# Performance work log

Measured on AMD Instinct MI355X. Metric: run time of the kernel, lower is better.

## Reference

```python
import jax, jax.numpy as jnp
import numpy as np

B, T, C, HS = 1024, 128, 384, 64


def setup_inputs() -> dict:
    key = jax.random.key(0)
    k1, k2, k3, k4 = jax.random.split(key, 4)
    std = 1.0 / np.sqrt(C)  # ~ nn.Linear default init scale
    return {
        "x": jax.random.normal(k1, (B, T, C), dtype=jnp.float32),
        "Wq": jax.random.normal(k2, (C, HS), dtype=jnp.float32) * std,
        "Wk": jax.random.normal(k3, (C, HS), dtype=jnp.float32) * std,
        "Wv": jax.random.normal(k4, (C, HS), dtype=jnp.float32) * std,
    }


def reference(x, Wq, Wk, Wv):
    # x: [B, T, C]; Wq/Wk/Wv: [C, HS]
    q = jnp.einsum("btc,ch->bth", x, Wq)
    k = jnp.einsum("btc,ch->bth", x, Wk)
    v = jnp.einsum("btc,ch->bth", x, Wv)
    scale = 1.0 / jnp.sqrt(jnp.asarray(k.shape[-1], dtype=x.dtype))
    wei = jnp.einsum("bth,bsh->bts", q, k) * scale  # [B, T, T]
    t = x.shape[1]
    causal = jnp.tril(jnp.ones((t, t), dtype=bool))
    wei = jnp.where(causal, wei, jnp.asarray(-jnp.inf, dtype=wei.dtype))
    wei = jax.nn.softmax(wei, axis=-1)
    # dropout omitted (eval mode / deterministic reference)
    out = jnp.einsum("bts,bsh->bth", wei, v)  # [B, T, HS]
    return out
```

## Files before the change

### kernel.cpp

```cpp
#include <hip/hip_runtime.h>


typedef __attribute__((ext_vector_type(8)))  short  short8;
typedef __attribute__((ext_vector_type(16))) float  floatx16;
typedef __attribute__((ext_vector_type(4)))  float  float4v;

#define T_DIM   128
#define C_DIM   384
#define HS      64
#define NCHUNK  12
#define SLAB    1536

#define QK_PITCH 68
#define V_PITCH  132
#define P_PITCH  132
#define Q_OFF 0
#define K_OFF 17408
#define V_OFF 34816
#define LDS_BYTES 51712
#define P_OFF 0
#define XS_OFF 0
#define XS_BUF 16384

#define MFMA(a,b,c) __builtin_amdgcn_mfma_f32_32x32x16_bf16((a),(b),(c),0,0,0)

__device__ inline unsigned short f2bf(float f){
    unsigned u = __builtin_bit_cast(unsigned, f);
    u += 0x7FFFu + ((u >> 16) & 1u);
    return (unsigned short)(u >> 16);
}

__device__ inline short8 ld_b64x2(const char* p){
    union { unsigned long long u[2]; short8 s; } r;
    r.u[0] = *(const unsigned long long*)(p);
    r.u[1] = *(const unsigned long long*)(p + 8);
    return r.s;
}

__global__ void prep_wt(const float* __restrict__ Wq, const float* __restrict__ Wk,
                        const float* __restrict__ Wv, unsigned short* __restrict__ wt){
    int idx = blockIdx.x * 256 + threadIdx.x;
    if (idx >= 48 * SLAB) return;
    int slab = idx / SLAB;
    int rem  = idx - slab * SLAB;
    int n = rem >> 3, j = rem & 7;
    int half = slab & 1, ks = (slab >> 1) & 1, c = slab >> 2;
    int kg = c*32 + ks*16 + half*8 + j;
    const float* W = (n < 64) ? Wq : (n < 128) ? Wk : Wv;
    wt[idx] = f2bf(W[kg * HS + (n & 63)]);
}

__launch_bounds__(256, 2)
__global__ void attn_kernel(const float* __restrict__ x,
                            const unsigned short* __restrict__ wtg,
                            float* __restrict__ out){
    __shared__ __align__(16) char smem[LDS_BYTES];
    const int tid  = threadIdx.x;
    const int lane = tid & 63;
    const int wave = tid >> 6;
    const int l31  = lane & 31;
    const int half = lane >> 5;
    const int koff = half * 8;
    const int b    = blockIdx.x;
    const float* xb = x + (size_t)b * (T_DIM * C_DIM);

    const int mpair = wave & 1;
    const int ntri  = wave >> 1;
    const short8* wf = (const short8*)wtg;
    const int nbase = 96 * ntri + l31;

    const char* xsrc = (const char*)xb
                     + (lane >> 3) * (C_DIM * 4)
                     + ((((lane & 7) ^ (lane >> 3))) << 4);

    auto stage = [&](int c, int sb){
        #pragma unroll
        for (int i = 0; i < 4; ++i){
            const char* g = xsrc + (i*4 + wave) * (8 * C_DIM * 4) + c * 128;
            char*       l = smem + XS_OFF + sb * XS_BUF + (i*4 + wave) * 1024;
            __builtin_amdgcn_global_load_lds(
                (const __attribute__((address_space(1))) unsigned*)g,
                (__attribute__((address_space(3))) unsigned*)l,
                16, 0, 0);
        }
    };

    floatx16 acc[6] = {};
    short8 bfr[2][2][3];

    #pragma unroll
    for (int ks = 0; ks < 2; ++ks)
        #pragma unroll
        for (int nbl = 0; nbl < 3; ++nbl)
            bfr[0][ks][nbl] = wf[((0*2 + ks)*2 + half)*192 + nbase + 32*nbl];
    stage(0, 0);
    stage(1, 1);
    asm volatile("s_waitcnt vmcnt(4)" ::: "memory");
    __builtin_amdgcn_s_barrier();
    asm volatile("" ::: "memory");

    #pragma unroll
    for (int c = 0; c < NCHUNK; ++c){
        if (c + 1 < NCHUNK){
            #pragma unroll
            for (int ks = 0; ks < 2; ++ks)
                #pragma unroll
                for (int nbl = 0; nbl < 3; ++nbl)
                    bfr[(c+1)&1][ks][nbl] =
                        wf[(((c+1)*2 + ks)*2 + half)*192 + nbase + 32*nbl];
        }
        if (c + 2 < NCHUNK) stage(c + 2, (c + 2) % 3);

        const char* sbuf = smem + XS_OFF + (c % 3) * XS_BUF;
        short8 afr[2][2];
        #pragma unroll
        for (int mbl = 0; mbl < 2; ++mbl){
            const int R  = 64*mpair + 32*mbl + l31;
            const char* rp = sbuf + R * 128;
            const int sw = (R & 7) << 4;
            #pragma unroll
            for (int ks = 0; ks < 2; ++ks){
                const int cb = ks*64 + half*32;
                float4v lo = *(const float4v*)(rp + ((cb     ) ^ sw));
                float4v hi = *(const float4v*)(rp + ((cb + 16) ^ sw));
                short8 a;
                a[0]=(short)f2bf(lo[0]); a[1]=(short)f2bf(lo[1]);
                a[2]=(short)f2bf(lo[2]); a[3]=(short)f2bf(lo[3]);
                a[4]=(short)f2bf(hi[0]); a[5]=(short)f2bf(hi[1]);
                a[6]=(short)f2bf(hi[2]); a[7]=(short)f2bf(hi[3]);
                afr[ks][mbl] = a;
            }
        }
        #pragma unroll
        for (int ks = 0; ks < 2; ++ks)
            #pragma unroll
            for (int nbl = 0; nbl < 3; ++nbl){
                acc[nbl*2+0] = MFMA(afr[ks][0], bfr[c&1][ks][nbl], acc[nbl*2+0]);
                acc[nbl*2+1] = MFMA(afr[ks][1], bfr[c&1][ks][nbl], acc[nbl*2+1]);
            }

        if (c + 1 < NCHUNK){
            if (c < NCHUNK - 2) asm volatile("s_waitcnt vmcnt(10)" ::: "memory");
            else                asm volatile("s_waitcnt vmcnt(6)"  ::: "memory");
            __builtin_amdgcn_s_barrier();
            asm volatile("" ::: "memory");
        }
    }
    __syncthreads();

    const float QSCALE = 0.125f * 1.44269504088896f;
    #pragma unroll
    for (int nbl = 0; nbl < 3; ++nbl)
        #pragma unroll
        for (int mbl = 0; mbl < 2; ++mbl){
            floatx16 A = acc[nbl*2+mbl];
            int nb = 3*ntri + nbl;
            int mb = 2*mpair + mbl;
            if (nb < 4){
                int base  = (nb < 2) ? Q_OFF : K_OFF;
                int col   = 32 * (nb & 1) + l31;
                float sc  = (nb < 2) ? QSCALE : 1.0f;
                char* bp  = smem + base + col * 2;
                #pragma unroll
                for (int r = 0; r < 16; ++r){
                    int t = 32*mb + (r&3) + 8*(r>>2) + 4*half;
                    *(unsigned short*)(bp + t * (QK_PITCH*2)) = f2bf(A[r] * sc);
                }
            } else {
                int h = 32*(nb-4) + l31;
                char* bp = smem + V_OFF + h * (V_PITCH*2);
                #pragma unroll
                for (int g = 0; g < 4; ++g){
                    int t0 = 32*mb + 8*g + 4*half;
                    union { unsigned short s[4]; unsigned long long u; } pk;
                    pk.s[0]=f2bf(A[4*g+0]); pk.s[1]=f2bf(A[4*g+1]);
                    pk.s[2]=f2bf(A[4*g+2]); pk.s[3]=f2bf(A[4*g+3]);
                    *(unsigned long long*)(bp + t0*2) = pk.u;
                }
            }
        }
    __syncthreads();

    floatx16 accS[4] = {};
    #pragma unroll
    for (int ks = 0; ks < 4; ++ks){
        short8 aq = ld_b64x2(smem + Q_OFF + (32*wave + l31)*(QK_PITCH*2) + (ks*16 + koff)*2);
        #pragma unroll
        for (int st = 0; st < 4; ++st)
            if (st <= wave){
                short8 bk = ld_b64x2(smem + K_OFF + (32*st + l31)*(QK_PITCH*2) + (ks*16 + koff)*2);
                accS[st] = MFMA(aq, bk, accS[st]);
            }
    }
    #pragma unroll
    for (int st = 0; st < 4; ++st)
        if (st <= wave){
            #pragma unroll
            for (int r = 0; r < 16; ++r){
                int trow = (r&3) + 8*(r>>2) + 4*half;
                float e = exp2f(accS[st][r]);
                if (st == wave && l31 > trow) e = 0.0f;
                accS[st][r] = e;
            }
        }

    float linv[16];
    #pragma unroll
    for (int r = 0; r < 16; ++r){
        float l = accS[0][r] + accS[1][r] + accS[2][r] + accS[3][r];
        #pragma unroll
        for (int m = 1; m <= 16; m <<= 1)
            l += __shfl_xor(l, m);
        linv[r] = 1.0f / l;
    }
    __syncthreads();

    #pragma unroll
    for (int st = 0; st < 4; ++st)
        if (st <= wave){
            char* bp = smem + P_OFF + (32*st + l31) * 2;
            #pragma unroll
            for (int r = 0; r < 16; ++r){
                int t = 32*wave + (r&3) + 8*(r>>2) + 4*half;
                *(unsigned short*)(bp + t * (P_PITCH*2)) = f2bf(accS[st][r]);
            }
        }
    __syncthreads();

    floatx16 accO0 = {}, accO1 = {};
    const int nks = 2 * (wave + 1);
    #pragma unroll
    for (int ks = 0; ks < 8; ++ks)
        if (ks < nks){
            short8 ap  = ld_b64x2(smem + P_OFF + (32*wave + l31)*(P_PITCH*2) + (ks*16 + koff)*2);
            short8 bv0 = ld_b64x2(smem + V_OFF + l31        *(V_PITCH*2) + (ks*16 + koff)*2);
            short8 bv1 = ld_b64x2(smem + V_OFF + (l31 + 32) *(V_PITCH*2) + (ks*16 + koff)*2);
            accO0 = MFMA(ap, bv0, accO0);
            accO1 = MFMA(ap, bv1, accO1);
        }

    float* ob = out + (size_t)b * (T_DIM * HS);
    #pragma unroll
    for (int r = 0; r < 16; ++r){
        int t = 32*wave + (r&3) + 8*(r>>2) + 4*half;
        ob[t*HS + l31]      = accO0[r] * linv[r];
        ob[t*HS + l31 + 32] = accO1[r] * linv[r];
    }
}

extern "C" void kernel_launch(void* const* d_in, const int* in_sizes, int n_in,
                              void* d_out, int out_size, void* d_ws, size_t ws_size,
                              hipStream_t stream){
    const float* x  = (const float*)d_in[0];
    const float* Wq = (const float*)d_in[1];
    const float* Wk = (const float*)d_in[2];
    const float* Wv = (const float*)d_in[3];
    unsigned short* wt = (unsigned short*)d_ws;

    prep_wt<<<288, 256, 0, stream>>>(Wq, Wk, Wv, wt);
    attn_kernel<<<1024, 256, 0, stream>>>(x, wt, (float*)d_out);
}
```

Measured before the change: 304.6 us.

## Stage x through registers and store bf16 tiles in double-buffered LDS

Replaces the async global_load_lds staging of fp32 x chunks (triple-buffered) with register-staged global loads. The data is converted to bf16 once and written to a padded, double-buffered LDS tile. The MFMA A-fragments are then read straight from LDS as bf16, with no per-wave fp32-to-bf16 conversion. This removes conversion work that waves sharing rows used to repeat, and roughly halves LDS traffic and footprint for the projection. In exchange it gives up the asynchronous direct-to-LDS path: each iteration now has a register round-trip and a conversion-plus-store before the barrier, which may expose global load latency.

```diff
diff --git a/kernel.cpp b/kernel.cpp
--- a/kernel.cpp
+++ b/kernel.cpp
@@ -20,7 +20,8 @@
 #define LDS_BYTES 51712
 #define P_OFF 0
 #define XS_OFF 0
-#define XS_BUF 16384
+#define XS_BUF 10240
+#define XP    80
 
 #define MFMA(a,b,c) __builtin_amdgcn_mfma_f32_32x32x16_bf16((a),(b),(c),0,0,0)
 
@@ -69,38 +70,46 @@
     const short8* wf = (const short8*)wtg;
     const int nbase = 96 * ntri + l31;
 
-    const char* xsrc = (const char*)xb
-                     + (lane >> 3) * (C_DIM * 4)
-                     + ((((lane & 7) ^ (lane >> 3))) << 4);
-
-    auto stage = [&](int c, int sb){
-        #pragma unroll
-        for (int i = 0; i < 4; ++i){
-            const char* g = xsrc + (i*4 + wave) * (8 * C_DIM * 4) + c * 128;
-            char*       l = smem + XS_OFF + sb * XS_BUF + (i*4 + wave) * 1024;
-            __builtin_amdgcn_global_load_lds(
-                (const __attribute__((address_space(1))) unsigned*)g,
-                (__attribute__((address_space(3))) unsigned*)l,
-                16, 0, 0);
-        }
+    const int srow  = tid >> 1;
+    const int shalf = tid & 1;
+    char* const bw0 = smem + XS_OFF + srow * XP + shalf * 32;
+
+    float4v ldreg[2][4];
+    auto xload = [&](int c, int s){
+        const float4v* g = (const float4v*)(xb + srow * C_DIM + c * 32 + shalf * 16);
+        ldreg[s][0] = g[0]; ldreg[s][1] = g[1];
+        ldreg[s][2] = g[2]; ldreg[s][3] = g[3];
+    };
+    auto cw = [&](int s, int sb){
+        short8 o0, o1;
+        #pragma unroll
+        for (int j = 0; j < 8; ++j){
+            o0[j] = (short)f2bf(ldreg[s][j >> 2    ][j & 3]);
+            o1[j] = (short)f2bf(ldreg[s][(j >> 2)+2][j & 3]);
+        }
+        char* p = bw0 + sb * XS_BUF;
+        *(short8*)(p)      = o0;
+        *(short8*)(p + 16) = o1;
     };
 
     floatx16 acc[6] = {};
     short8 bfr[2][2][3];
 
+    xload(0, 0);
+    xload(1, 1);
     #pragma unroll
     for (int ks = 0; ks < 2; ++ks)
         #pragma unroll
         for (int nbl = 0; nbl < 3; ++nbl)
             bfr[0][ks][nbl] = wf[((0*2 + ks)*2 + half)*192 + nbase + 32*nbl];
-    stage(0, 0);
-    stage(1, 1);
-    asm volatile("s_waitcnt vmcnt(4)" ::: "memory");
+    cw(0, 0);
+    asm volatile("s_waitcnt lgkmcnt(0)" ::: "memory");
     __builtin_amdgcn_s_barrier();
     asm volatile("" ::: "memory");
 
     #pragma unroll
     for (int c = 0; c < NCHUNK; ++c){
+        if (c + 2 < NCHUNK) xload(c + 2, c & 1);
         if (c + 1 < NCHUNK){
             #pragma unroll
             for (int ks = 0; ks < 2; ++ks)
@@ -109,27 +118,15 @@
                     bfr[(c+1)&1][ks][nbl] =
                         wf[(((c+1)*2 + ks)*2 + half)*192 + nbase + 32*nbl];
         }
-        if (c + 2 < NCHUNK) stage(c + 2, (c + 2) % 3);
-
-        const char* sbuf = smem + XS_OFF + (c % 3) * XS_BUF;
+
+        const char* sbuf = smem + XS_OFF + (c & 1) * XS_BUF;
         short8 afr[2][2];
         #pragma unroll
         for (int mbl = 0; mbl < 2; ++mbl){
-            const int R  = 64*mpair + 32*mbl + l31;
-            const char* rp = sbuf + R * 128;
-            const int sw = (R & 7) << 4;
-            #pragma unroll
-            for (int ks = 0; ks < 2; ++ks){
-                const int cb = ks*64 + half*32;
-                float4v lo = *(const float4v*)(rp + ((cb     ) ^ sw));
-                float4v hi = *(const float4v*)(rp + ((cb + 16) ^ sw));
-                short8 a;
-                a[0]=(short)f2bf(lo[0]); a[1]=(short)f2bf(lo[1]);
-                a[2]=(short)f2bf(lo[2]); a[3]=(short)f2bf(lo[3]);
-                a[4]=(short)f2bf(hi[0]); a[5]=(short)f2bf(hi[1]);
-                a[6]=(short)f2bf(hi[2]); a[7]=(short)f2bf(hi[3]);
-                afr[ks][mbl] = a;
-            }
+            const int R = 64*mpair + 32*mbl + l31;
+            #pragma unroll
+            for (int ks = 0; ks < 2; ++ks)
+                afr[ks][mbl] = *(const short8*)(sbuf + R * XP + ks*32 + half*16);
         }
         #pragma unroll
         for (int ks = 0; ks < 2; ++ks)
@@ -140,8 +137,8 @@
             }
 
         if (c + 1 < NCHUNK){
-            if (c < NCHUNK - 2) asm volatile("s_waitcnt vmcnt(10)" ::: "memory");
-            else                asm volatile("s_waitcnt vmcnt(6)"  ::: "memory");
+            cw((c+1)&1, (c+1)&1);
+            asm volatile("s_waitcnt lgkmcnt(0)" ::: "memory");
             __builtin_amdgcn_s_barrier();
             asm volatile("" ::: "memory");
         }
```

Result: no change. 304.4 us (-0.1%).
